# Optimization experiments

Hardware: AMD Instinct MI355X
Metric: run time of the kernel (lower is better)

The kernel has to match this reference:

```python
import jax, jax.numpy as jnp
import numpy as np

E, D_MODEL, D_HIDDEN, N_TOKENS = 8, 1024, 4096, 16384


def setup_inputs() -> dict:
    key = jax.random.key(0)
    ks = jax.random.split(key, 6)
    inp = {
        "hidden_states": jax.random.normal(ks[0], (N_TOKENS, D_MODEL), jnp.float32),
        # tokens are pre-sorted by expert; equal-sized groups of N_TOKENS // E
        "fwd_expert_count": jnp.full((E,), N_TOKENS // E, dtype=jnp.int32),
        # weights stored [E, d_in, d_out] (math-equivalent transpose of torch's [E, out, in])
        "w_gelu": jax.random.normal(ks[1], (E, D_MODEL, D_HIDDEN), jnp.float32) * 0.02,
        "w_lin": jax.random.normal(ks[2], (E, D_MODEL, D_HIDDEN), jnp.float32) * 0.02,
        "b_lin": jax.random.normal(ks[3], (E, D_HIDDEN), jnp.float32) * 0.02,
        "w_o": jax.random.normal(ks[4], (E, D_HIDDEN, D_MODEL), jnp.float32) * 0.02,
        "b_o": jax.random.normal(ks[5], (E, D_MODEL), jnp.float32) * 0.02,
    }
    return inp


def reference(hidden_states, fwd_expert_count, w_gelu, w_lin, b_lin, w_o, b_o):
    # Grouped GEMM MoE expert FFN with gated GELU (T5DenseGatedActDense per expert).
    # setup_inputs uses equal group sizes, so the grouped GEMM is expressed as a
    # batched einsum over [E, capacity, d] blocks (tokens are sorted by expert).
    e, d_model, d_hidden = w_gelu.shape
    n = hidden_states.shape[0]
    cap = n // e  # per-expert token count (== fwd_expert_count[i])
    x = hidden_states.reshape(e, cap, d_model)
    # gate branch: no bias (FMoELinear bias=False), gelu_new (tanh approx)
    hidden_gelu = jax.nn.gelu(jnp.einsum('ecd,edh->ech', x, w_gelu), approximate=True)
    # linear branch: bias=True
    hidden_linear = jnp.einsum('ecd,edh->ech', x, w_lin) + b_lin[:, None, :]
    h = hidden_gelu * hidden_linear  # dropout is identity at inference
    out = jnp.einsum('ech,ehd->ecd', h, w_o) + b_o[:, None, :]
    return out.reshape(n, d_model)
```

## Files before the change

### kernel.cpp

```cpp
#include <hip/hip_runtime.h>

#define EXP 8
#define DM 1024
#define DH 4096
#define NT 16384

typedef __attribute__((ext_vector_type(8))) short bf16x8;
typedef __attribute__((ext_vector_type(4))) float f32x4;

static __device__ __forceinline__ unsigned short f2bf(float f) {
  unsigned int u = __float_as_uint(f);
  u = u + 0x7FFFu + ((u >> 16) & 1u);
  return (unsigned short)(u >> 16);
}

static __device__ __forceinline__ void gload_lds16(const void* g, void* l) {
  __builtin_amdgcn_global_load_lds((const __attribute__((address_space(1))) void*)g,
                                   (__attribute__((address_space(3))) void*)l, 16, 0, 0);
}

static __device__ __forceinline__ int swz_idx(int r, int kk) {
  return r * 64 + (((kk >> 3) ^ (r & 7)) << 3);
}

__global__ void cvt_bf16_k(const float* __restrict__ in, unsigned short* __restrict__ out,
                           long n4) {
  long i = (long)blockIdx.x * blockDim.x + threadIdx.x;
  const long stride = (long)gridDim.x * blockDim.x;
  for (; i < n4; i += stride) {
    const float4 v = ((const float4*)in)[i];
    ushort4 o;
    o.x = f2bf(v.x); o.y = f2bf(v.y); o.z = f2bf(v.z); o.w = f2bf(v.w);
    ((ushort4*)out)[i] = o;
  }
}

__global__ void transpose_cvt(const float* __restrict__ in, unsigned short* __restrict__ out,
                              int K, int N) {
  __shared__ float tile[32][33];
  const int n0 = blockIdx.x * 32, k0 = blockIdx.y * 32;
  const size_t boff = (size_t)blockIdx.z * K * N;
  const int tx = threadIdx.x, ty = threadIdx.y;
  const float* src = in + boff;
  unsigned short* dst = out + boff;
#pragma unroll
  for (int i = 0; i < 32; i += 8)
    tile[ty + i][tx] = src[(size_t)(k0 + ty + i) * N + n0 + tx];
  __syncthreads();
#pragma unroll
  for (int i = 0; i < 32; i += 8)
    dst[(size_t)(n0 + ty + i) * K + k0 + tx] = f2bf(tile[tx][ty + i]);
}

__global__ __launch_bounds__(256, 2) void gemm1(
    const unsigned short* __restrict__ Xb,
    const unsigned short* __restrict__ WgT,
    const unsigned short* __restrict__ WlT,
    const float* __restrict__ b_lin,
    unsigned short* __restrict__ Hb) {
  __shared__ unsigned short sA[128 * 64];
  __shared__ unsigned short sBg[128 * 64];
  __shared__ unsigned short sBl[128 * 64];

  const int t = threadIdx.x;
  const int nblk = blockIdx.x, mblk = blockIdx.y;
  const int e = mblk >> 4;
  const int m0 = mblk * 128, n0 = nblk * 128;

  const int lane = t & 63;
  const int wave = t >> 6;
  const int wr = wave >> 1, wc = wave & 1;
  const int lrow = lane & 15;
  const int lk8 = (lane >> 4) * 8;

  const int srow = t >> 3;
  const int schunk = t & 7;
  const int ssw = ((schunk ^ (srow & 7)) << 3);

  const unsigned short* gA = Xb + (size_t)m0 * DM + ssw;
  const unsigned short* gG = WgT + (size_t)e * DH * DM + (size_t)n0 * DM + ssw;
  const unsigned short* gL = WlT + (size_t)e * DH * DM + (size_t)n0 * DM + ssw;

  f32x4 accg[4][4], accl[4][4];
#pragma unroll
  for (int i = 0; i < 4; i++)
#pragma unroll
    for (int j = 0; j < 4; j++) { accg[i][j] = 0.0f; accl[i][j] = 0.0f; }

  for (int kt = 0; kt < DM / 64; ++kt) {
    const int k0 = kt * 64;
#pragma unroll
    for (int c = 0; c < 4; c++) {
      const int row = c * 32 + srow;
      gload_lds16(gA + (size_t)row * DM + k0, (char*)sA + row * 128 + schunk * 16);
      gload_lds16(gG + (size_t)row * DM + k0, (char*)sBg + row * 128 + schunk * 16);
      gload_lds16(gL + (size_t)row * DM + k0, (char*)sBl + row * 128 + schunk * 16);
    }
    __syncthreads();
#pragma unroll
    for (int ks = 0; ks < 2; ks++) {
      const int kk = ks * 32 + lk8;
      bf16x8 af[4], bg[4], bl[4];
#pragma unroll
      for (int i = 0; i < 4; i++)
        af[i] = *(const bf16x8*)&sA[swz_idx(wr * 64 + i * 16 + lrow, kk)];
#pragma unroll
      for (int j = 0; j < 4; j++) {
        bg[j] = *(const bf16x8*)&sBg[swz_idx(wc * 64 + j * 16 + lrow, kk)];
        bl[j] = *(const bf16x8*)&sBl[swz_idx(wc * 64 + j * 16 + lrow, kk)];
      }
#pragma unroll
      for (int i = 0; i < 4; i++)
#pragma unroll
        for (int j = 0; j < 4; j++) {
          accg[i][j] = __builtin_amdgcn_mfma_f32_16x16x32_bf16(af[i], bg[j], accg[i][j], 0, 0, 0);
          accl[i][j] = __builtin_amdgcn_mfma_f32_16x16x32_bf16(af[i], bl[j], accl[i][j], 0, 0, 0);
        }
    }
    __syncthreads();
  }

  const float* bl_p = b_lin + (size_t)e * DH;
  const int r0 = (lane >> 4) * 4;
#pragma unroll
  for (int i = 0; i < 4; i++) {
    const int grow = m0 + wr * 64 + i * 16 + r0;
#pragma unroll
    for (int j = 0; j < 4; j++) {
      const int gcol = n0 + wc * 64 + j * 16 + lrow;
      const float bias = bl_p[gcol];
#pragma unroll
      for (int r = 0; r < 4; r++) {
        const float g = accg[i][j][r];
        const float li = accl[i][j][r] + bias;
        const float u = 0.7978845608028654f * (g + 0.044715f * g * g * g);
        const float th = 1.0f - 2.0f / (1.0f + __expf(2.0f * u));
        const float h = 0.5f * g * (1.0f + th) * li;
        Hb[(size_t)(grow + r) * DH + gcol] = f2bf(h);
      }
    }
  }
}


#define LDSA(row, chunk) lds[sb + (row) * 64 + ((((chunk) ^ ((row) & 7))) << 3)]
#define LDSB(row, chunk) lds[sb + 16384 + (row) * 64 + ((((chunk) ^ ((row) & 7))) << 3)]

#define RD_A(mh)                                                                   \
  _Pragma("unroll") for (int i = 0; i < 4; i++) _Pragma("unroll") for (int ks = 0; \
                                                                       ks < 2;    \
                                                                       ks++)      \
      fa[i][ks] = *(const bf16x8*)&LDSA(wr * 128 + (mh) * 64 + i * 16 + lrow, ks * 4 + khi);

#define RD_B(dst, jb)                                                              \
  _Pragma("unroll") for (int j = 0; j < 2; j++) _Pragma("unroll") for (int ks = 0; \
                                                                       ks < 2;    \
                                                                       ks++)      \
      dst[j][ks] = *(const bf16x8*)&LDSB(wc * 64 + ((jb) + j) * 16 + lrow, ks * 4 + khi);

#define MFMA16(mi, jb, fb)                                                        \
  __builtin_amdgcn_s_setprio(1);                                                  \
  _Pragma("unroll") for (int i = 0; i < 4; i++) _Pragma("unroll") for (int j = 0; \
                                                                       j < 2;    \
                                                                       j++)      \
      _Pragma("unroll") for (int ks = 0; ks < 2; ks++) acc[(mi) + i][(jb) + j] =  \
          __builtin_amdgcn_mfma_f32_16x16x32_bf16(fa[i][ks], fb[j][ks],           \
                                                  acc[(mi) + i][(jb) + j], 0, 0, 0); \
  __builtin_amdgcn_s_setprio(0);

#define BAR_FENCE()                      \
  __builtin_amdgcn_s_barrier();          \
  asm volatile("" ::: "memory");

__global__ __launch_bounds__(512, 1) void gemm2(
    const unsigned short* __restrict__ Hb,
    const unsigned short* __restrict__ WoT,
    const float* __restrict__ b_o,
    float* __restrict__ out) {
  __shared__ unsigned short lds[65536];

  const int t = threadIdx.x;
  const int nblk = blockIdx.x, mblk = blockIdx.y;
  const int e = mblk >> 3;
  const int m0 = mblk * 256, n0 = nblk * 256;

  const int lane = t & 63, wave = t >> 6;
  const int wr = wave >> 2, wc = wave & 3;
  const int lrow = lane & 15, khi = lane >> 4;

  const int presw = (((t & 7) ^ ((t >> 3) & 7)) << 3);
  const unsigned short* gAsrc = Hb + (size_t)(m0 + (t >> 3)) * DH + presw;
  const unsigned short* gBsrc = WoT + ((size_t)e * DM + n0 + (t >> 3)) * DH + presw;

  const int KT = DH / 64;

  auto STAGE_A = [&](int kt, int half) {
    unsigned short* d = &lds[(kt & 1) * 32768 + half * 8192 + t * 8];
    const unsigned short* s = gAsrc + (size_t)(half * 128) * DH + kt * 64;
    gload_lds16(s, d);
    gload_lds16(s + (size_t)64 * DH, d + 4096);
  };
  auto STAGE_B = [&](int kt, int half) {
    unsigned short* d = &lds[(kt & 1) * 32768 + 16384 + half * 8192 + t * 8];
    const unsigned short* s = gBsrc + (size_t)(half * 128) * DH + kt * 64;
    gload_lds16(s, d);
    gload_lds16(s + (size_t)64 * DH, d + 4096);
  };

  f32x4 acc[8][4];
#pragma unroll
  for (int m = 0; m < 8; m++)
#pragma unroll
    for (int j = 0; j < 4; j++) acc[m][j] = 0.0f;

  STAGE_A(0, 0); STAGE_A(0, 1);
  STAGE_B(0, 0); STAGE_B(0, 1);
  STAGE_B(1, 0); STAGE_B(1, 1);
  asm volatile("s_waitcnt vmcnt(4)" ::: "memory");
  BAR_FENCE();

  for (int T = 0; T < KT; ++T) {
    const int sb = (T & 1) * 32768;
    bf16x8 fa[4][2], fb01[2][2], fb23[2][2];
    RD_A(0);
    RD_B(fb01, 0);
    if (T + 1 < KT) STAGE_A(T + 1, 0);
    __builtin_amdgcn_s_barrier();
    MFMA16(0, 0, fb01);
    BAR_FENCE();
    RD_B(fb23, 2);
    if (T + 1 < KT) STAGE_A(T + 1, 1);
    __builtin_amdgcn_s_barrier();
    MFMA16(0, 2, fb23);
    BAR_FENCE();
    RD_A(1);
    if (T + 2 < KT) STAGE_B(T + 2, 0);
    __builtin_amdgcn_s_barrier();
    MFMA16(4, 2, fb23);
    BAR_FENCE();
    if (T + 2 < KT) STAGE_B(T + 2, 1);
    __builtin_amdgcn_s_barrier();
    MFMA16(4, 0, fb01);
    if (T < KT - 2)       asm volatile("s_waitcnt vmcnt(4)" ::: "memory");
    else if (T == KT - 2) asm volatile("s_waitcnt vmcnt(0)" ::: "memory");
    BAR_FENCE();
  }

  const float* bop = b_o + (size_t)e * DM;
#pragma unroll
  for (int m = 0; m < 8; m++) {
    const int rowbase = m0 + wr * 128 + (m >> 2) * 64 + (m & 3) * 16 + khi * 4;
#pragma unroll
    for (int j = 0; j < 4; j++) {
      const int gcol = n0 + wc * 64 + j * 16 + lrow;
      const float bias = bop[gcol];
#pragma unroll
      for (int r = 0; r < 4; r++)
        out[(size_t)(rowbase + r) * DM + gcol] = acc[m][j][r] + bias;
    }
  }
}

extern "C" void kernel_launch(void* const* d_in, const int* in_sizes, int n_in,
                              void* d_out, int out_size, void* d_ws, size_t ws_size,
                              hipStream_t stream) {
  const float* hs = (const float*)d_in[0];
  const float* w_gelu = (const float*)d_in[2];
  const float* w_lin = (const float*)d_in[3];
  const float* b_lin = (const float*)d_in[4];
  const float* w_o = (const float*)d_in[5];
  const float* b_o = (const float*)d_in[6];
  float* outp = (float*)d_out;

  unsigned short* Xb = (unsigned short*)d_ws;
  unsigned short* WgT = Xb + (size_t)NT * DM;
  unsigned short* WlT = WgT + (size_t)EXP * DH * DM;
  unsigned short* WoT = WlT + (size_t)EXP * DH * DM;
  unsigned short* Hb = WoT + (size_t)EXP * DH * DM;

  cvt_bf16_k<<<dim3(2048), dim3(256), 0, stream>>>(hs, Xb, (long)NT * DM / 4);
  transpose_cvt<<<dim3(DH / 32, DM / 32, EXP), dim3(32, 8), 0, stream>>>(w_gelu, WgT, DM, DH);
  transpose_cvt<<<dim3(DH / 32, DM / 32, EXP), dim3(32, 8), 0, stream>>>(w_lin, WlT, DM, DH);
  transpose_cvt<<<dim3(DM / 32, DH / 32, EXP), dim3(32, 8), 0, stream>>>(w_o, WoT, DH, DM);

  gemm1<<<dim3(DH / 128, NT / 128), dim3(256), 0, stream>>>(Xb, WgT, WlT, b_lin, Hb);
  gemm2<<<dim3(DM / 256, NT / 256), dim3(512), 0, stream>>>(Hb, WoT, b_o, outp);
}
```

Baseline: 588.7 us.

## Vectorize weight transpose with 64x64 tiles, merge launches, remap GEMM blocks per XCD

Replaces the 32x32 scalar transpose-convert with a 64x64 tile version that uses float4 loads and ushort4 stores. It also merges the gate and linear weight transposes into one launch. Both GEMMs now remap the linear block id so that consecutive blocks dispatched round-robin across the 8 XCDs land on contiguous tiles, which should improve L2 reuse of the shared weight and activation tiles. The larger LDS tile and the strided column reads in the transpose may add bank conflicts.

```diff
diff --git a/kernel.cpp b/kernel.cpp
--- a/kernel.cpp
+++ b/kernel.cpp
@@ -35,21 +35,34 @@
   }
 }
 
-__global__ void transpose_cvt(const float* __restrict__ in, unsigned short* __restrict__ out,
-                              int K, int N) {
-  __shared__ float tile[32][33];
-  const int n0 = blockIdx.x * 32, k0 = blockIdx.y * 32;
-  const size_t boff = (size_t)blockIdx.z * K * N;
-  const int tx = threadIdx.x, ty = threadIdx.y;
-  const float* src = in + boff;
-  unsigned short* dst = out + boff;
-#pragma unroll
-  for (int i = 0; i < 32; i += 8)
-    tile[ty + i][tx] = src[(size_t)(k0 + ty + i) * N + n0 + tx];
+__global__ void transpose_cvt64(const float* __restrict__ srcA, const float* __restrict__ srcB,
+                                unsigned short* __restrict__ dstA,
+                                unsigned short* __restrict__ dstB, int K, int N) {
+  __shared__ float tile[64][65];
+  const int t = threadIdx.x;
+  const int tx = t & 15, ty = t >> 4;
+  const int n0 = blockIdx.x * 64, k0 = blockIdx.y * 64;
+  const int z = blockIdx.z;
+  const float* src = (z >> 3 ? srcB : srcA) + (size_t)(z & 7) * K * N;
+  unsigned short* dst = (z >> 3 ? dstB : dstA) + (size_t)(z & 7) * K * N;
+#pragma unroll
+  for (int i = 0; i < 64; i += 16) {
+    const float4 v = *(const float4*)&src[(size_t)(k0 + ty + i) * N + n0 + tx * 4];
+    tile[ty + i][tx * 4 + 0] = v.x;
+    tile[ty + i][tx * 4 + 1] = v.y;
+    tile[ty + i][tx * 4 + 2] = v.z;
+    tile[ty + i][tx * 4 + 3] = v.w;
+  }
   __syncthreads();
 #pragma unroll
-  for (int i = 0; i < 32; i += 8)
-    dst[(size_t)(n0 + ty + i) * K + k0 + tx] = f2bf(tile[tx][ty + i]);
+  for (int i = 0; i < 64; i += 16) {
+    ushort4 o;
+    o.x = f2bf(tile[tx * 4 + 0][ty + i]);
+    o.y = f2bf(tile[tx * 4 + 1][ty + i]);
+    o.z = f2bf(tile[tx * 4 + 2][ty + i]);
+    o.w = f2bf(tile[tx * 4 + 3][ty + i]);
+    *(ushort4*)&dst[(size_t)(n0 + ty + i) * K + k0 + tx * 4] = o;
+  }
 }
 
 __global__ __launch_bounds__(256, 2) void gemm1(
@@ -63,7 +76,9 @@
   __shared__ unsigned short sBl[128 * 64];
 
   const int t = threadIdx.x;
-  const int nblk = blockIdx.x, mblk = blockIdx.y;
+  const int bid = blockIdx.x + (int)gridDim.x * blockIdx.y;
+  const int nb = (bid & 7) * 512 + (bid >> 3);
+  const int nblk = nb & 31, mblk = nb >> 5;
   const int e = mblk >> 4;
   const int m0 = mblk * 128, n0 = nblk * 128;
 
@@ -180,7 +195,9 @@
   __shared__ unsigned short lds[65536];
 
   const int t = threadIdx.x;
-  const int nblk = blockIdx.x, mblk = blockIdx.y;
+  const int bid = blockIdx.x + (int)gridDim.x * blockIdx.y;
+  const int nb = (bid & 7) * 32 + (bid >> 3);
+  const int nblk = nb & 3, mblk = nb >> 2;
   const int e = mblk >> 3;
   const int m0 = mblk * 256, n0 = nblk * 256;
 
@@ -279,9 +296,10 @@
   unsigned short* Hb = WoT + (size_t)EXP * DH * DM;
 
   cvt_bf16_k<<<dim3(2048), dim3(256), 0, stream>>>(hs, Xb, (long)NT * DM / 4);
-  transpose_cvt<<<dim3(DH / 32, DM / 32, EXP), dim3(32, 8), 0, stream>>>(w_gelu, WgT, DM, DH);
-  transpose_cvt<<<dim3(DH / 32, DM / 32, EXP), dim3(32, 8), 0, stream>>>(w_lin, WlT, DM, DH);
-  transpose_cvt<<<dim3(DM / 32, DH / 32, EXP), dim3(32, 8), 0, stream>>>(w_o, WoT, DH, DM);
+  transpose_cvt64<<<dim3(DH / 64, DM / 64, 16), dim3(256), 0, stream>>>(
+      w_gelu, w_lin, WgT, WlT, DM, DH);
+  transpose_cvt64<<<dim3(DM / 64, DH / 64, 8), dim3(256), 0, stream>>>(
+      w_o, w_o, WoT, WoT, DH, DM);
 
   gemm1<<<dim3(DH / 128, NT / 128), dim3(256), 0, stream>>>(Xb, WgT, WlT, b_lin, Hb);
   gemm2<<<dim3(DM / 256, NT / 256), dim3(512), 0, stream>>>(Hb, WoT, b_o, outp);
```

Result: slower. 606.7 us (+3.1%).
